# Kernel optimization log

Hardware: AMD Instinct MI355X
Metric: run time of the kernel (lower is better)

## Reference

```python
import jax, jax.numpy as jnp
import numpy as np

# Constants from the torch module __init__
FACE_INDS = np.array([[0, 1, 2, 3], [0, 4, 2, 6], [0, 1, 4, 5],
                      [1, 3, 5, 7], [2, 3, 6, 7], [4, 5, 6, 7]])  # (6,4)
N_GRID = 11
N_POINTS = N_GRID * N_GRID        # 121
N_FACE = 6
N_KP_HAND = 21
N_CONTACTS = 10
ITA = 0.2
IND1 = np.array([0, 1, 2, 3])
IND2 = np.array([1, 2, 3, 0])


def _bilinear_grid():
    # grid[p, k] = bilinear weights for the 4 face corners, p over 11x11 (u,v)
    g = []
    for u in np.linspace(0.0, 1.0, N_GRID):
        for v in np.linspace(0.0, 1.0, N_GRID):
            g.append([v * (1 - u), v * u, (1 - v) * (1 - u), u * (1 - v)])
    return jnp.asarray(np.array(g, dtype=np.float32))  # (121, 4)


def setup_inputs() -> dict:
    key = jax.random.key(0)
    poses = jax.random.normal(key, (8192, N_KP_HAND + 8, 3), dtype=jnp.float32)
    return {"poses": poses}


def affinity_loss(poses):
    bs = poses.shape[0]
    hand = poses[:, :N_KP_HAND, :]          # (bs, 21, 3)
    obj = poses[:, N_KP_HAND:, :]           # (bs, 8, 3)

    # --- sample_face_points: bilinear sample 121 pts on each of the 6 faces ---
    grid = _bilinear_grid().astype(poses.dtype)        # (121, 4)
    faces = obj[:, FACE_INDS, :]                        # (bs, 6, 4, 3)
    face_points = jnp.einsum('bfkc,pk->bfpc', faces, grid)  # (bs, 6, 121, 3)
    obj_pts = face_points.reshape(bs, N_FACE * N_POINTS, 3)  # (bs, 726, 3)

    xx = jnp.sum(hand * hand, axis=-1)                  # (bs, 21)
    yy = jnp.sum(obj_pts * obj_pts, axis=-1)            # (bs, 726)
    zz = jnp.einsum('bic,bjc->bij', hand, obj_pts)      # (bs, 21, 726)
    pdist = jnp.sqrt(xx[:, :, None] + yy[:, None, :] - 2.0 * zz + 1e-6)
    pdist = pdist.reshape(bs, N_KP_HAND, N_FACE, N_POINTS)

    # --- per (hand kp, face) nearest face point, then global top-10 contacts ---
    dist_h2f = jnp.min(pdist, axis=3)                   # (bs, 21, 6)
    idxs_h2f = jnp.argmin(pdist, axis=3)                # (bs, 21, 6)
    flat = dist_h2f.reshape(bs, N_KP_HAND * N_FACE)     # (bs, 126)
    order = jnp.argsort(flat, axis=1)[:, :N_CONTACTS]   # (bs, 10)
    dist = jnp.take_along_axis(flat, order, axis=1)     # (bs, 10)
    inds_hand = order // N_FACE
    inds_face = order % N_FACE
    b = jnp.arange(bs)[:, None]
    ind_obj = idxs_h2f[b, inds_hand, inds_face]                     # (bs, 10)
    obj_contacts = obj_pts[b, inds_face * N_POINTS + ind_obj]       # (bs, 10, 3)

    # --- get_obj_info: axis endpoints and mean edge length of the bbox ---
    points1 = obj[:, :4, :].mean(axis=1)                # (bs, 3)
    points2 = obj[:, 4:, :].mean(axis=1)                # (bs, 3)
    l1 = jnp.linalg.norm(obj[:, IND1] - obj[:, IND2], axis=-1).mean(1, keepdims=True)
    l2 = jnp.linalg.norm(obj[:, IND1 + 4] - obj[:, IND2 + 4], axis=-1).mean(1, keepdims=True)
    length = (l1 + l2) * 0.5                            # (bs, 1)

    mask1 = (dist < length * ITA).astype(poses.dtype)   # (bs, 10)
    mask = mask1[:, :, None] * mask1[:, None, :]        # (bs, 10, 10)

    direct_vec = points2 - points1                      # (bs, 3)
    dv_norm = jnp.linalg.norm(direct_vec, axis=1, keepdims=True)  # (bs, 1)
    normed_dv = direct_vec / (dv_norm + 1e-5)
    vec_contacts = obj_contacts - points1[:, None, :]   # (bs, 10, 3)
    inner = jnp.sum(direct_vec[:, None, :] * vec_contacts, axis=-1)  # (bs, 10)
    t = inner / (dv_norm + 1e-5)                        # (bs, 10)
    r = points1[:, None, :] + normed_dv[:, None, :] * t[:, :, None]  # (bs, 10, 3)
    normal_vec = obj_contacts - r
    normal_vec = normal_vec / (jnp.linalg.norm(normal_vec, axis=2, keepdims=True) + 1e-5)
    cos_sim = jnp.einsum('bic,bjc->bij', normal_vec, normal_vec)  # (bs, 10, 10)

    return (cos_sim * mask).sum() / (mask.sum() + 1.0)


def reference(poses):
    return affinity_loss(poses)
```

## Files before the change

### kernel.cpp

```cpp
#include <hip/hip_runtime.h>
#include <math.h>

#define NGRID   11
#define NPAIR   126
#define NCONT   10

#define NSUB    64
#define NBUK    128
#define WS_SUB  16
#define WS_BUK  128
#define WS_WORDS (WS_BUK + 2 * NBUK)

#define NBUCKET 256

__device__ __constant__ int4 c_face4[6] = {
    {0,1,2,3},{0,4,2,6},{0,1,4,5},{1,3,5,7},{2,3,6,7},{4,5,6,7}};
__device__ __constant__ float c_U[NGRID] = {
    0.0f,0.1f,0.2f,0.3f,0.4f,0.5f,0.6f,0.7f,0.8f,0.9f,1.0f};

__global__ void zero_ws_kernel(float* ws, int n) {
    int t = blockIdx.x * 256 + threadIdx.x;
    if (t < n) ws[t] = 0.0f;
}

__device__ __forceinline__ void pair_coefs(
        const float* __restrict__ obj, float hx, float hy, float hz, int f,
        float& C00, float& C10, float& C01, float& C11,
        float& C20, float& C02, float& C21, float& C12, float& C22) {
    const int4 F = c_face4[f];
    float C0[3], C1[3], C2[3], C3[3];
    #pragma unroll
    for (int c = 0; c < 3; ++c) {
        C0[c] = obj[F.x * 3 + c];
        C1[c] = obj[F.y * 3 + c];
        C2[c] = obj[F.z * 3 + c];
        C3[c] = obj[F.w * 3 + c];
    }
    float av[3], bv[3], cv[3], dv[3];
    #pragma unroll
    for (int c = 0; c < 3; ++c) {
        av[c] = C2[c];
        bv[c] = C3[c] - C2[c];
        cv[c] = C0[c] - C2[c];
        dv[c] = C1[c] - C0[c] - C3[c] + C2[c];
    }
    float aa = 0.f, bb = 0.f, cc = 0.f, dd = 0.f;
    float ab = 0.f, ac = 0.f, ad = 0.f, bc = 0.f, bd = 0.f, cd = 0.f;
    #pragma unroll
    for (int c = 0; c < 3; ++c) {
        aa += av[c] * av[c]; bb += bv[c] * bv[c];
        cc += cv[c] * cv[c]; dd += dv[c] * dv[c];
        ab += av[c] * bv[c]; ac += av[c] * cv[c];
        ad += av[c] * dv[c]; bc += bv[c] * cv[c];
        bd += bv[c] * dv[c]; cd += cv[c] * dv[c];
    }
    const float hx2 = 2.0f * hx, hy2 = 2.0f * hy, hz2 = 2.0f * hz;
    const float ha2 = fmaf(hx2, av[0], fmaf(hy2, av[1], hz2 * av[2]));
    const float hb2 = fmaf(hx2, bv[0], fmaf(hy2, bv[1], hz2 * bv[2]));
    const float hc2 = fmaf(hx2, cv[0], fmaf(hy2, cv[1], hz2 * cv[2]));
    const float hd2 = fmaf(hx2, dv[0], fmaf(hy2, dv[1], hz2 * dv[2]));
    C00 = ha2 - aa;
    C10 = hb2 - 2.f * ab;
    C01 = hc2 - 2.f * ac;
    C11 = hd2 - 2.f * (ad + bc);
    C20 = -bb;  C02 = -cc;  C21 = -2.f * bd;  C12 = -2.f * cd;  C22 = -dd;
}

__launch_bounds__(256)
__global__ void affinity_kernel(const float* __restrict__ poses,
                                float* __restrict__ ws,
                                float* __restrict__ out,
                                int bs, int mode) {
    const int t    = threadIdx.x;
    const int half = t >> 7;
    const int t0   = t & 127;
    const int batch = blockIdx.x * 2 + half;
    const bool valid = batch < bs;

    __shared__ float sh_pose[2][88];
    __shared__ __align__(16) unsigned sh_key[2][128];
    __shared__ int   sh_ru[2][128];
    __shared__ int   sh_ch[2][NCONT];
    __shared__ float sh_ctr[2][NCONT][4];
    __shared__ float sh_nd[2][2];
    __shared__ int    sh_last;
    __shared__ double sh_rn[4], sh_rd[4];

    if (valid && t0 < 87) sh_pose[half][t0] = poses[(size_t)batch * 87 + t0];
    __syncthreads();

    const float* hand = sh_pose[half];
    const float* obj  = sh_pose[half] + 63;

    if (t0 >= NPAIR) sh_key[half][t0] = 0xFFFFFFFFu;
    if (valid && t0 < NPAIR) {
        const int i = t0 / 6;
        const int f = t0 - i * 6;
        const float hx = hand[i * 3 + 0], hy = hand[i * 3 + 1], hz = hand[i * 3 + 2];
        const float xx = hx * hx + hy * hy + hz * hz;
        float C00, C10, C01, C11, C20, C02, C21, C12, C22;
        pair_coefs(obj, hx, hy, hz, f, C00, C10, C01, C11, C20, C02, C21, C12, C22);

        const float U[NGRID] = {0.0f,0.1f,0.2f,0.3f,0.4f,0.5f,
                                0.6f,0.7f,0.8f,0.9f,1.0f};
        float qb = -3.0e38f;
        int   ru = 0;
        #pragma unroll
        for (int iu = 0; iu < NGRID; ++iu) {
            const float u  = U[iu];
            const float A2 = fmaf(fmaf(C22, u, C12), u, C02);
            const float A1 = fmaf(fmaf(C21, u, C11), u, C01);
            const float A0 = fmaf(fmaf(C20, u, C10), u, C00);
            float qr = A0;
            #pragma unroll
            for (int iv = 1; iv < NGRID; ++iv) {
                qr = fmaxf(qr, fmaf(fmaf(A2, U[iv], A1), U[iv], A0));
            }
            if (qr > qb) { qb = qr; ru = iu; }
        }
        float d2 = fmaxf(xx - qb, 0.0f);
        sh_key[half][t0] = (__float_as_uint(d2) & 0xFFFFFF80u) | (unsigned)t0;
        sh_ru[half][t0]  = ru;
    }
    __syncthreads();

    if (valid && t0 < NPAIR) {
        const unsigned ki = sh_key[half][t0];
        const uint4* kp = (const uint4*)sh_key[half];
        int rank = 0;
        #pragma unroll 8
        for (int j = 0; j < 32; ++j) {
            const uint4 v = kp[j];
            rank += (v.x < ki) + (v.y < ki) + (v.z < ki) + (v.w < ki);
        }
        if (rank < NCONT) sh_ch[half][rank] = t0;
    }
    __syncthreads();

    if (valid && t0 < NCONT) {
        const int ci = sh_ch[half][t0];
        const int i  = ci / 6;
        const int f  = ci - 6 * i;
        const int ru = sh_ru[half][ci];
        const float hx = hand[i * 3 + 0], hy = hand[i * 3 + 1], hz = hand[i * 3 + 2];

        float C00, C10, C01, C11, C20, C02, C21, C12, C22;
        pair_coefs(obj, hx, hy, hz, f, C00, C10, C01, C11, C20, C02, C21, C12, C22);
        const float u  = c_U[ru];
        const float A2 = fmaf(fmaf(C22, u, C12), u, C02);
        const float A1 = fmaf(fmaf(C21, u, C11), u, C01);
        const float A0 = fmaf(fmaf(C20, u, C10), u, C00);
        const float U[NGRID] = {0.0f,0.1f,0.2f,0.3f,0.4f,0.5f,
                                0.6f,0.7f,0.8f,0.9f,1.0f};
        float qr = A0;
        int   vb = 0;
        #pragma unroll
        for (int iv = 1; iv < NGRID; ++iv) {
            const float q = fmaf(fmaf(A2, U[iv], A1), U[iv], A0);
            if (q > qr) { qr = q; vb = iv; }
        }

        const double du = ru * 0.1;
        const double dv = vb * 0.1;
        const float w0 = (float)(dv * (1.0 - du));
        const float w1 = (float)(dv * du);
        const float w2 = (float)((1.0 - dv) * (1.0 - du));
        const float w3 = (float)(du * (1.0 - dv));
        const int4 F = c_face4[f];
        const int i0 = F.x * 3, i1 = F.y * 3, i2 = F.z * 3, i3 = F.w * 3;
        const float cx = w0 * obj[i0 + 0] + w1 * obj[i1 + 0]
                       + w2 * obj[i2 + 0] + w3 * obj[i3 + 0];
        const float cy = w0 * obj[i0 + 1] + w1 * obj[i1 + 1]
                       + w2 * obj[i2 + 1] + w3 * obj[i3 + 1];
        const float cz = w0 * obj[i0 + 2] + w1 * obj[i1 + 2]
                       + w2 * obj[i2 + 2] + w3 * obj[i3 + 2];

        const float xx = hx * hx + hy * hy + hz * hz;
        const float yy = cx * cx + cy * cy + cz * cz;
        const float zz = hx * cx + hy * cy + hz * cz;
        const float dist = sqrtf(((xx + yy) - 2.0f * zz) + 1e-6f);

        float p1x = (((obj[0]  + obj[3])  + obj[6])  + obj[9])  * 0.25f;
        float p1y = (((obj[1]  + obj[4])  + obj[7])  + obj[10]) * 0.25f;
        float p1z = (((obj[2]  + obj[5])  + obj[8])  + obj[11]) * 0.25f;
        float p2x = (((obj[12] + obj[15]) + obj[18]) + obj[21]) * 0.25f;
        float p2y = (((obj[13] + obj[16]) + obj[19]) + obj[22]) * 0.25f;
        float p2z = (((obj[14] + obj[17]) + obj[20]) + obj[23]) * 0.25f;

        float l1 = 0.0f, l2 = 0.0f;
        #pragma unroll
        for (int e = 0; e < 4; ++e) {
            const int a = e, b2 = (e + 1) & 3;
            {
                const float dx = obj[a * 3 + 0] - obj[b2 * 3 + 0];
                const float dy = obj[a * 3 + 1] - obj[b2 * 3 + 1];
                const float dz = obj[a * 3 + 2] - obj[b2 * 3 + 2];
                l1 += sqrtf(dx * dx + dy * dy + dz * dz);
            }
            {
                const float dx = obj[(a + 4) * 3 + 0] - obj[(b2 + 4) * 3 + 0];
                const float dy = obj[(a + 4) * 3 + 1] - obj[(b2 + 4) * 3 + 1];
                const float dz = obj[(a + 4) * 3 + 2] - obj[(b2 + 4) * 3 + 2];
                l2 += sqrtf(dx * dx + dy * dy + dz * dz);
            }
        }
        l1 *= 0.25f; l2 *= 0.25f;
        const float length = (l1 + l2) * 0.5f;
        const float m = (dist < length * 0.2f) ? 1.0f : 0.0f;

        const float dvx = p2x - p1x, dvy = p2y - p1y, dvz = p2z - p1z;
        const float dvn = sqrtf(dvx * dvx + dvy * dvy + dvz * dvz);
        const float den = dvn + 1e-5f;
        const float ndx = dvx / den, ndy = dvy / den, ndz = dvz / den;
        const float vcx = cx - p1x, vcy = cy - p1y, vcz = cz - p1z;
        const float inner = dvx * vcx + dvy * vcy + dvz * vcz;
        const float tp = inner / den;
        const float rx = p1x + ndx * tp, ry = p1y + ndy * tp, rz = p1z + ndz * tp;
        float nvx = cx - rx, nvy = cy - ry, nvz = cz - rz;
        const float nvn = sqrtf(nvx * nvx + nvy * nvy + nvz * nvz) + 1e-5f;
        nvx /= nvn; nvy /= nvn; nvz /= nvn;

        sh_ctr[half][t0][0] = m * nvx;
        sh_ctr[half][t0][1] = m * nvy;
        sh_ctr[half][t0][2] = m * nvz;
        sh_ctr[half][t0][3] = m;
    }
    __syncthreads();

    if (t0 == 0) {
        float num = 0.f, dnm = 0.f;
        if (valid) {
            float sx = 0.f, sy = 0.f, sz = 0.f, sk = 0.f;
            #pragma unroll
            for (int c = 0; c < NCONT; ++c) {
                sx += sh_ctr[half][c][0]; sy += sh_ctr[half][c][1];
                sz += sh_ctr[half][c][2]; sk += sh_ctr[half][c][3];
            }
            num = sx * sx + sy * sy + sz * sz;
            dnm = sk * sk;
        }
        sh_nd[half][0] = num;
        sh_nd[half][1] = dnm;
    }
    __syncthreads();

    if (t == 0) {
        sh_last = 0;
        const float num = sh_nd[0][0] + sh_nd[1][0];
        const float dnm = sh_nd[0][1] + sh_nd[1][1];
        const int b = blockIdx.x;
        if (mode) {
            float* bkt = ws + WS_BUK + 2 * (b & (NBUK - 1));
            const float r0 = atomicAdd(bkt + 0, num);
            const float r1 = atomicAdd(bkt + 1, dnm);
            asm volatile("" :: "v"(r0), "v"(r1) : "memory");
            unsigned* subs = (unsigned*)ws + WS_SUB;
            const unsigned nb = gridDim.x;
            const unsigned g  = (unsigned)b & (NSUB - 1);
            const unsigned quota = (nb - 1u - g) / NSUB + 1u;
            const unsigned old = atomicAdd(subs + g, 1u);
            if (old + 1u == quota) {
                const unsigned ngroups = nb < NSUB ? nb : NSUB;
                const unsigned m2 = atomicAdd((unsigned*)ws, 1u);
                if (m2 + 1u == ngroups) sh_last = 1;
            }
        } else {
            float* bucket = ws + 2 * (b & (NBUCKET - 1));
            atomicAdd(bucket + 0, num);
            atomicAdd(bucket + 1, dnm);
        }
    }
    __syncthreads();

    if (sh_last) {
        double n = 0.0, d = 0.0;
        if (t < NBUK) {
            float* bkt = ws + WS_BUK + 2 * t;
            n = (double)atomicAdd(bkt + 0, 0.0f);
            d = (double)atomicAdd(bkt + 1, 0.0f);
        }
        #pragma unroll
        for (int off = 32; off >= 1; off >>= 1) {
            n += __shfl_xor(n, off, 64);
            d += __shfl_xor(d, off, 64);
        }
        const int w = t >> 6;
        if ((t & 63) == 0) { sh_rn[w] = n; sh_rd[w] = d; }
        __syncthreads();
        if (t == 0) {
            const double nn = sh_rn[0] + sh_rn[1] + sh_rn[2] + sh_rn[3];
            const double dd = sh_rd[0] + sh_rd[1] + sh_rd[2] + sh_rd[3];
            out[0] = (float)(nn / (dd + 1.0));
        }
    }
}

__launch_bounds__(1024)
__global__ void finalize_kernel(const float* __restrict__ ws,
                                float* __restrict__ out, int nslot) {
    const int t = threadIdx.x;
    __shared__ double sh_n[16], sh_d[16];
    double n = 0.0, d = 0.0;
    for (int k = t; k < nslot; k += 1024) {
        n += (double)ws[2 * k + 0];
        d += (double)ws[2 * k + 1];
    }
    #pragma unroll
    for (int off = 32; off >= 1; off >>= 1) {
        n += __shfl_xor(n, off, 64);
        d += __shfl_xor(d, off, 64);
    }
    const int w = t >> 6;
    if ((t & 63) == 0) { sh_n[w] = n; sh_d[w] = d; }
    __syncthreads();
    if (t == 0) {
        double nn = 0.0, dd = 0.0;
        #pragma unroll
        for (int i = 0; i < 16; ++i) { nn += sh_n[i]; dd += sh_d[i]; }
        out[0] = (float)(nn / (dd + 1.0));
    }
}

extern "C" void kernel_launch(void* const* d_in, const int* in_sizes, int n_in,
                              void* d_out, int out_size, void* d_ws, size_t ws_size,
                              hipStream_t stream) {
    const float* poses = (const float*)d_in[0];
    float* out = (float*)d_out;
    float* ws  = (float*)d_ws;
    const int bs = in_sizes[0] / 87;
    const int nblk = (bs + 1) / 2;

    if (ws_size >= (size_t)WS_WORDS * sizeof(float)) {
        hipMemsetAsync(ws, 0, WS_WORDS * sizeof(float), stream);
        hipLaunchKernelGGL(affinity_kernel, dim3(nblk), dim3(256), 0, stream,
                           poses, ws, out, bs, 1);
    } else {
        hipLaunchKernelGGL(zero_ws_kernel, dim3(1), dim3(256), 0, stream,
                           ws, NBUCKET * 2);
        hipLaunchKernelGGL(affinity_kernel, dim3(nblk), dim3(256), 0, stream,
                           poses, ws, out, bs, 0);
        hipLaunchKernelGGL(finalize_kernel, dim3(1), dim3(1024), 0, stream,
                           ws, out, NBUCKET);
    }
}
```

Baseline: 82.58 us.

## Precompute per-face coefficients, packed-FMA grid search, and threshold-filter contact candidates

Per-face quadratic coefficients are computed once per batch by six threads and stored in shared memory instead of being recomputed by every pair thread. The 11x11 grid scan now evaluates two u rows at a time with packed float2 FMA and max. Pairs whose approximate squared distance exceeds the contact threshold are dropped early, so only survivors get refined, ranked among themselves and reduced. The final sum uses a wavefront shuffle instead of a serial loop. The filter depends on a heuristic slack term and changes the ranking structure, which could affect correctness at threshold edges.

```diff
diff --git a/kernel.cpp b/kernel.cpp
--- a/kernel.cpp
+++ b/kernel.cpp
@@ -13,6 +13,11 @@
 
 #define NBUCKET 256
 
+typedef float v2f __attribute__((ext_vector_type(2)));
+#define FMA2(a,b,c) __builtin_elementwise_fma((a),(b),(c))
+#define MAX2(a,b)   __builtin_elementwise_max((a),(b))
+#define SP2(x)      ((v2f){(x),(x)})
+
 __device__ __constant__ int4 c_face4[6] = {
     {0,1,2,3},{0,4,2,6},{0,1,4,5},{1,3,5,7},{2,3,6,7},{4,5,6,7}};
 __device__ __constant__ float c_U[NGRID] = {
@@ -23,47 +28,22 @@
     if (t < n) ws[t] = 0.0f;
 }
 
-__device__ __forceinline__ void pair_coefs(
-        const float* __restrict__ obj, float hx, float hy, float hz, int f,
+__device__ __forceinline__ void coefs_from_face(
+        const float4* __restrict__ Ff, float hx, float hy, float hz,
         float& C00, float& C10, float& C01, float& C11,
         float& C20, float& C02, float& C21, float& C12, float& C22) {
-    const int4 F = c_face4[f];
-    float C0[3], C1[3], C2[3], C3[3];
-    #pragma unroll
-    for (int c = 0; c < 3; ++c) {
-        C0[c] = obj[F.x * 3 + c];
-        C1[c] = obj[F.y * 3 + c];
-        C2[c] = obj[F.z * 3 + c];
-        C3[c] = obj[F.w * 3 + c];
-    }
-    float av[3], bv[3], cv[3], dv[3];
-    #pragma unroll
-    for (int c = 0; c < 3; ++c) {
-        av[c] = C2[c];
-        bv[c] = C3[c] - C2[c];
-        cv[c] = C0[c] - C2[c];
-        dv[c] = C1[c] - C0[c] - C3[c] + C2[c];
-    }
-    float aa = 0.f, bb = 0.f, cc = 0.f, dd = 0.f;
-    float ab = 0.f, ac = 0.f, ad = 0.f, bc = 0.f, bd = 0.f, cd = 0.f;
-    #pragma unroll
-    for (int c = 0; c < 3; ++c) {
-        aa += av[c] * av[c]; bb += bv[c] * bv[c];
-        cc += cv[c] * cv[c]; dd += dv[c] * dv[c];
-        ab += av[c] * bv[c]; ac += av[c] * cv[c];
-        ad += av[c] * dv[c]; bc += bv[c] * cv[c];
-        bd += bv[c] * dv[c]; cd += cv[c] * dv[c];
-    }
+    const float4 F0 = Ff[0], F1 = Ff[1], F2 = Ff[2],
+                 F3 = Ff[3], F4 = Ff[4], F5 = Ff[5];
     const float hx2 = 2.0f * hx, hy2 = 2.0f * hy, hz2 = 2.0f * hz;
-    const float ha2 = fmaf(hx2, av[0], fmaf(hy2, av[1], hz2 * av[2]));
-    const float hb2 = fmaf(hx2, bv[0], fmaf(hy2, bv[1], hz2 * bv[2]));
-    const float hc2 = fmaf(hx2, cv[0], fmaf(hy2, cv[1], hz2 * cv[2]));
-    const float hd2 = fmaf(hx2, dv[0], fmaf(hy2, dv[1], hz2 * dv[2]));
-    C00 = ha2 - aa;
-    C10 = hb2 - 2.f * ab;
-    C01 = hc2 - 2.f * ac;
-    C11 = hd2 - 2.f * (ad + bc);
-    C20 = -bb;  C02 = -cc;  C21 = -2.f * bd;  C12 = -2.f * cd;  C22 = -dd;
+    const float ha2 = fmaf(hx2, F0.x, fmaf(hy2, F0.y, hz2 * F0.z));
+    const float hb2 = fmaf(hx2, F1.x, fmaf(hy2, F1.y, hz2 * F1.z));
+    const float hc2 = fmaf(hx2, F2.x, fmaf(hy2, F2.y, hz2 * F2.z));
+    const float hd2 = fmaf(hx2, F3.x, fmaf(hy2, F3.y, hz2 * F3.z));
+    C00 = ha2 - F0.w;
+    C10 = hb2 - F4.x;
+    C01 = hc2 - F4.y;
+    C11 = hd2 - F4.z;
+    C20 = -F1.w;  C02 = -F2.w;  C21 = -F4.w;  C12 = -F5.x;  C22 = -F3.w;
 }
 
 __launch_bounds__(256)
@@ -77,170 +57,234 @@
     const int batch = blockIdx.x * 2 + half;
     const bool valid = batch < bs;
 
-    __shared__ float sh_pose[2][88];
-    __shared__ __align__(16) unsigned sh_key[2][128];
-    __shared__ int   sh_ru[2][128];
-    __shared__ int   sh_ch[2][NCONT];
-    __shared__ float sh_ctr[2][NCONT][4];
-    __shared__ float sh_nd[2][2];
-    __shared__ int    sh_last;
-    __shared__ double sh_rn[4], sh_rd[4];
+    __shared__ float    sh_pose[2][88];
+    __shared__ float4   sh_face[2][36];
+    __shared__ float    sh_thr[2][2];
+    __shared__ int      sh_ru[2][128];
+    __shared__ int      sh_cpair[2][128];
+    __shared__ unsigned sh_cnt[2], sh_cnt2[2];
+    __shared__ unsigned sh_key[2][128];
+    __shared__ float    sh_cont[2][128][3];
+    __shared__ float    sh_win[2][NCONT][3];
+    __shared__ float    sh_nd[2][2];
+    __shared__ int      sh_last;
+    __shared__ double   sh_rn[4], sh_rd[4];
 
     if (valid && t0 < 87) sh_pose[half][t0] = poses[(size_t)batch * 87 + t0];
+    if (t0 == 127) { sh_cnt[half] = 0u; sh_cnt2[half] = 0u; }
     __syncthreads();
 
     const float* hand = sh_pose[half];
     const float* obj  = sh_pose[half] + 63;
 
-    if (t0 >= NPAIR) sh_key[half][t0] = 0xFFFFFFFFu;
+    if (valid && t0 < 6) {
+        const int4 F = c_face4[t0];
+        float C0[3], C1[3], C2[3], C3[3];
+        #pragma unroll
+        for (int c = 0; c < 3; ++c) {
+            C0[c] = obj[F.x * 3 + c];
+            C1[c] = obj[F.y * 3 + c];
+            C2[c] = obj[F.z * 3 + c];
+            C3[c] = obj[F.w * 3 + c];
+        }
+        float av[3], bv[3], cv[3], dv[3];
+        #pragma unroll
+        for (int c = 0; c < 3; ++c) {
+            av[c] = C2[c];
+            bv[c] = C3[c] - C2[c];
+            cv[c] = C0[c] - C2[c];
+            dv[c] = C1[c] - C0[c] - C3[c] + C2[c];
+        }
+        float aa=0.f,bb=0.f,cc=0.f,dd=0.f,ab=0.f,ac=0.f,ad=0.f,bc=0.f,bd=0.f,cd=0.f;
+        #pragma unroll
+        for (int c = 0; c < 3; ++c) {
+            aa += av[c]*av[c]; bb += bv[c]*bv[c];
+            cc += cv[c]*cv[c]; dd += dv[c]*dv[c];
+            ab += av[c]*bv[c]; ac += av[c]*cv[c];
+            ad += av[c]*dv[c]; bc += bv[c]*cv[c];
+            bd += bv[c]*dv[c]; cd += cv[c]*dv[c];
+        }
+        float4* Ff = &sh_face[half][t0 * 6];
+        Ff[0] = make_float4(av[0], av[1], av[2], aa);
+        Ff[1] = make_float4(bv[0], bv[1], bv[2], bb);
+        Ff[2] = make_float4(cv[0], cv[1], cv[2], cc);
+        Ff[3] = make_float4(dv[0], dv[1], dv[2], dd);
+        Ff[4] = make_float4(2.f*ab, 2.f*ac, 2.f*(ad+bc), 2.f*bd);
+        Ff[5] = make_float4(2.f*cd, 0.f, 0.f, 0.f);
+    }
+    if (valid && t0 == 6) {
+        float l1 = 0.0f, l2 = 0.0f;
+        #pragma unroll
+        for (int e = 0; e < 4; ++e) {
+            const int a = e, b2 = (e + 1) & 3;
+            {
+                const float dx = obj[a*3+0]-obj[b2*3+0];
+                const float dy = obj[a*3+1]-obj[b2*3+1];
+                const float dz = obj[a*3+2]-obj[b2*3+2];
+                l1 += sqrtf(dx*dx + dy*dy + dz*dz);
+            }
+            {
+                const float dx = obj[(a+4)*3+0]-obj[(b2+4)*3+0];
+                const float dy = obj[(a+4)*3+1]-obj[(b2+4)*3+1];
+                const float dz = obj[(a+4)*3+2]-obj[(b2+4)*3+2];
+                l2 += sqrtf(dx*dx + dy*dy + dz*dz);
+            }
+        }
+        l1 *= 0.25f; l2 *= 0.25f;
+        const float L02 = (l1 + l2) * 0.5f * 0.2f;
+        sh_thr[half][0] = L02 * L02 - 1e-6f + 1e-2f;
+        sh_thr[half][1] = L02;
+    }
+    __syncthreads();
+
     if (valid && t0 < NPAIR) {
         const int i = t0 / 6;
         const int f = t0 - i * 6;
-        const float hx = hand[i * 3 + 0], hy = hand[i * 3 + 1], hz = hand[i * 3 + 2];
-        const float xx = hx * hx + hy * hy + hz * hz;
-        float C00, C10, C01, C11, C20, C02, C21, C12, C22;
-        pair_coefs(obj, hx, hy, hz, f, C00, C10, C01, C11, C20, C02, C21, C12, C22);
+        const float hx = hand[i*3+0], hy = hand[i*3+1], hz = hand[i*3+2];
+        const float xx = hx*hx + hy*hy + hz*hz;
+        float C00,C10,C01,C11,C20,C02,C21,C12,C22;
+        coefs_from_face(&sh_face[half][f*6], hx, hy, hz,
+                        C00,C10,C01,C11,C20,C02,C21,C12,C22);
 
         const float U[NGRID] = {0.0f,0.1f,0.2f,0.3f,0.4f,0.5f,
                                 0.6f,0.7f,0.8f,0.9f,1.0f};
         float qb = -3.0e38f;
         int   ru = 0;
         #pragma unroll
-        for (int iu = 0; iu < NGRID; ++iu) {
-            const float u  = U[iu];
-            const float A2 = fmaf(fmaf(C22, u, C12), u, C02);
-            const float A1 = fmaf(fmaf(C21, u, C11), u, C01);
-            const float A0 = fmaf(fmaf(C20, u, C10), u, C00);
-            float qr = A0;
+        for (int rp = 0; rp < 5; ++rp) {
+            const v2f u2 = (v2f){U[2*rp], U[2*rp+1]};
+            const v2f A2 = FMA2(FMA2(SP2(C22), u2, SP2(C12)), u2, SP2(C02));
+            const v2f A1 = FMA2(FMA2(SP2(C21), u2, SP2(C11)), u2, SP2(C01));
+            const v2f A0 = FMA2(FMA2(SP2(C20), u2, SP2(C10)), u2, SP2(C00));
+            v2f m2 = A0;
             #pragma unroll
             for (int iv = 1; iv < NGRID; ++iv) {
-                qr = fmaxf(qr, fmaf(fmaf(A2, U[iv], A1), U[iv], A0));
-            }
-            if (qr > qb) { qb = qr; ru = iu; }
-        }
-        float d2 = fmaxf(xx - qb, 0.0f);
-        sh_key[half][t0] = (__float_as_uint(d2) & 0xFFFFFF80u) | (unsigned)t0;
-        sh_ru[half][t0]  = ru;
-    }
-    __syncthreads();
-
-    if (valid && t0 < NPAIR) {
-        const unsigned ki = sh_key[half][t0];
-        const uint4* kp = (const uint4*)sh_key[half];
+                const v2f vv = SP2(U[iv]);
+                m2 = MAX2(m2, FMA2(FMA2(A2, vv, A1), vv, A0));
+            }
+            if (m2.x > qb) { qb = m2.x; ru = 2*rp; }
+            if (m2.y > qb) { qb = m2.y; ru = 2*rp + 1; }
+        }
+        {
+            const float u = 1.0f;
+            const float A2 = fmaf(fmaf(C22,u,C12),u,C02);
+            const float A1 = fmaf(fmaf(C21,u,C11),u,C01);
+            const float A0 = fmaf(fmaf(C20,u,C10),u,C00);
+            float m1 = A0;
+            #pragma unroll
+            for (int iv = 1; iv < NGRID; ++iv)
+                m1 = fmaxf(m1, fmaf(fmaf(A2,U[iv],A1),U[iv],A0));
+            if (m1 > qb) { qb = m1; ru = 10; }
+        }
+        sh_ru[half][t0] = ru;
+        const float d2s = xx - qb;
+        if (d2s < sh_thr[half][0]) {
+            const unsigned s = atomicAdd(&sh_cnt[half], 1u);
+            sh_cpair[half][s] = t0;
+        }
+    }
+    __syncthreads();
+
+    {
+        const int cnt = (int)sh_cnt[half];
+        if (t0 < cnt) {
+            const int pair = sh_cpair[half][t0];
+            const int i  = pair / 6;
+            const int f  = pair - 6 * i;
+            const int ru = sh_ru[half][pair];
+            const float hx = hand[i*3+0], hy = hand[i*3+1], hz = hand[i*3+2];
+            float C00,C10,C01,C11,C20,C02,C21,C12,C22;
+            coefs_from_face(&sh_face[half][f*6], hx, hy, hz,
+                            C00,C10,C01,C11,C20,C02,C21,C12,C22);
+            const float u  = c_U[ru];
+            const float A2 = fmaf(fmaf(C22,u,C12),u,C02);
+            const float A1 = fmaf(fmaf(C21,u,C11),u,C01);
+            const float A0 = fmaf(fmaf(C20,u,C10),u,C00);
+            const float U[NGRID] = {0.0f,0.1f,0.2f,0.3f,0.4f,0.5f,
+                                    0.6f,0.7f,0.8f,0.9f,1.0f};
+            float qr = A0; int vb = 0;
+            #pragma unroll
+            for (int iv = 1; iv < NGRID; ++iv) {
+                const float q = fmaf(fmaf(A2,U[iv],A1),U[iv],A0);
+                if (q > qr) { qr = q; vb = iv; }
+            }
+            const double du = ru * 0.1;
+            const double dv = vb * 0.1;
+            const float w0 = (float)(dv * (1.0 - du));
+            const float w1 = (float)(dv * du);
+            const float w2 = (float)((1.0 - dv) * (1.0 - du));
+            const float w3 = (float)(du * (1.0 - dv));
+            const int4 F = c_face4[f];
+            const int i0 = F.x*3, i1 = F.y*3, i2 = F.z*3, i3 = F.w*3;
+            const float cx = w0*obj[i0+0]+w1*obj[i1+0]+w2*obj[i2+0]+w3*obj[i3+0];
+            const float cy = w0*obj[i0+1]+w1*obj[i1+1]+w2*obj[i2+1]+w3*obj[i3+1];
+            const float cz = w0*obj[i0+2]+w1*obj[i1+2]+w2*obj[i2+2]+w3*obj[i3+2];
+            const float xx = hx*hx + hy*hy + hz*hz;
+            const float yy = cx*cx + cy*cy + cz*cz;
+            const float zz = hx*cx + hy*cy + hz*cz;
+            const float d2e = (xx + yy) - 2.0f * zz;
+            const float dist = sqrtf(d2e + 1e-6f);
+            if (dist < sh_thr[half][1]) {
+                const unsigned s2 = atomicAdd(&sh_cnt2[half], 1u);
+                const float d2k = fmaxf(d2e, 0.0f);
+                sh_key[half][s2] = (__float_as_uint(d2k) & 0xFFFFFF80u)
+                                 | (unsigned)pair;
+                sh_cont[half][s2][0] = cx;
+                sh_cont[half][s2][1] = cy;
+                sh_cont[half][s2][2] = cz;
+            }
+        }
+    }
+    __syncthreads();
+
+    const int n2 = (int)sh_cnt2[half];
+    if (t0 < n2) {
+        const unsigned ke = sh_key[half][t0];
         int rank = 0;
-        #pragma unroll 8
-        for (int j = 0; j < 32; ++j) {
-            const uint4 v = kp[j];
-            rank += (v.x < ki) + (v.y < ki) + (v.z < ki) + (v.w < ki);
-        }
-        if (rank < NCONT) sh_ch[half][rank] = t0;
-    }
-    __syncthreads();
-
-    if (valid && t0 < NCONT) {
-        const int ci = sh_ch[half][t0];
-        const int i  = ci / 6;
-        const int f  = ci - 6 * i;
-        const int ru = sh_ru[half][ci];
-        const float hx = hand[i * 3 + 0], hy = hand[i * 3 + 1], hz = hand[i * 3 + 2];
-
-        float C00, C10, C01, C11, C20, C02, C21, C12, C22;
-        pair_coefs(obj, hx, hy, hz, f, C00, C10, C01, C11, C20, C02, C21, C12, C22);
-        const float u  = c_U[ru];
-        const float A2 = fmaf(fmaf(C22, u, C12), u, C02);
-        const float A1 = fmaf(fmaf(C21, u, C11), u, C01);
-        const float A0 = fmaf(fmaf(C20, u, C10), u, C00);
-        const float U[NGRID] = {0.0f,0.1f,0.2f,0.3f,0.4f,0.5f,
-                                0.6f,0.7f,0.8f,0.9f,1.0f};
-        float qr = A0;
-        int   vb = 0;
-        #pragma unroll
-        for (int iv = 1; iv < NGRID; ++iv) {
-            const float q = fmaf(fmaf(A2, U[iv], A1), U[iv], A0);
-            if (q > qr) { qr = q; vb = iv; }
-        }
-
-        const double du = ru * 0.1;
-        const double dv = vb * 0.1;
-        const float w0 = (float)(dv * (1.0 - du));
-        const float w1 = (float)(dv * du);
-        const float w2 = (float)((1.0 - dv) * (1.0 - du));
-        const float w3 = (float)(du * (1.0 - dv));
-        const int4 F = c_face4[f];
-        const int i0 = F.x * 3, i1 = F.y * 3, i2 = F.z * 3, i3 = F.w * 3;
-        const float cx = w0 * obj[i0 + 0] + w1 * obj[i1 + 0]
-                       + w2 * obj[i2 + 0] + w3 * obj[i3 + 0];
-        const float cy = w0 * obj[i0 + 1] + w1 * obj[i1 + 1]
-                       + w2 * obj[i2 + 1] + w3 * obj[i3 + 1];
-        const float cz = w0 * obj[i0 + 2] + w1 * obj[i1 + 2]
-                       + w2 * obj[i2 + 2] + w3 * obj[i3 + 2];
-
-        const float xx = hx * hx + hy * hy + hz * hz;
-        const float yy = cx * cx + cy * cy + cz * cz;
-        const float zz = hx * cx + hy * cy + hz * cz;
-        const float dist = sqrtf(((xx + yy) - 2.0f * zz) + 1e-6f);
-
-        float p1x = (((obj[0]  + obj[3])  + obj[6])  + obj[9])  * 0.25f;
-        float p1y = (((obj[1]  + obj[4])  + obj[7])  + obj[10]) * 0.25f;
-        float p1z = (((obj[2]  + obj[5])  + obj[8])  + obj[11]) * 0.25f;
-        float p2x = (((obj[12] + obj[15]) + obj[18]) + obj[21]) * 0.25f;
-        float p2y = (((obj[13] + obj[16]) + obj[19]) + obj[22]) * 0.25f;
-        float p2z = (((obj[14] + obj[17]) + obj[20]) + obj[23]) * 0.25f;
-
-        float l1 = 0.0f, l2 = 0.0f;
-        #pragma unroll
-        for (int e = 0; e < 4; ++e) {
-            const int a = e, b2 = (e + 1) & 3;
-            {
-                const float dx = obj[a * 3 + 0] - obj[b2 * 3 + 0];
-                const float dy = obj[a * 3 + 1] - obj[b2 * 3 + 1];
-                const float dz = obj[a * 3 + 2] - obj[b2 * 3 + 2];
-                l1 += sqrtf(dx * dx + dy * dy + dz * dz);
-            }
-            {
-                const float dx = obj[(a + 4) * 3 + 0] - obj[(b2 + 4) * 3 + 0];
-                const float dy = obj[(a + 4) * 3 + 1] - obj[(b2 + 4) * 3 + 1];
-                const float dz = obj[(a + 4) * 3 + 2] - obj[(b2 + 4) * 3 + 2];
-                l2 += sqrtf(dx * dx + dy * dy + dz * dz);
-            }
-        }
-        l1 *= 0.25f; l2 *= 0.25f;
-        const float length = (l1 + l2) * 0.5f;
-        const float m = (dist < length * 0.2f) ? 1.0f : 0.0f;
-
-        const float dvx = p2x - p1x, dvy = p2y - p1y, dvz = p2z - p1z;
-        const float dvn = sqrtf(dvx * dvx + dvy * dvy + dvz * dvz);
+        for (int j = 0; j < n2; ++j) rank += (sh_key[half][j] < ke) ? 1 : 0;
+        if (rank < NCONT) {
+            sh_win[half][rank][0] = sh_cont[half][t0][0];
+            sh_win[half][rank][1] = sh_cont[half][t0][1];
+            sh_win[half][rank][2] = sh_cont[half][t0][2];
+        }
+    }
+    __syncthreads();
+
+    const int kwin = n2 < NCONT ? n2 : NCONT;
+    float px = 0.f, py = 0.f, pz = 0.f;
+    if (valid && t0 < kwin) {
+        const float cx = sh_win[half][t0][0];
+        const float cy = sh_win[half][t0][1];
+        const float cz = sh_win[half][t0][2];
+        const float p1x = (((obj[0] +obj[3]) +obj[6]) +obj[9]) *0.25f;
+        const float p1y = (((obj[1] +obj[4]) +obj[7]) +obj[10])*0.25f;
+        const float p1z = (((obj[2] +obj[5]) +obj[8]) +obj[11])*0.25f;
+        const float p2x = (((obj[12]+obj[15])+obj[18])+obj[21])*0.25f;
+        const float p2y = (((obj[13]+obj[16])+obj[19])+obj[22])*0.25f;
+        const float p2z = (((obj[14]+obj[17])+obj[20])+obj[23])*0.25f;
+        const float dvx = p2x-p1x, dvy = p2y-p1y, dvz = p2z-p1z;
+        const float dvn = sqrtf(dvx*dvx + dvy*dvy + dvz*dvz);
         const float den = dvn + 1e-5f;
-        const float ndx = dvx / den, ndy = dvy / den, ndz = dvz / den;
-        const float vcx = cx - p1x, vcy = cy - p1y, vcz = cz - p1z;
-        const float inner = dvx * vcx + dvy * vcy + dvz * vcz;
+        const float ndx = dvx/den, ndy = dvy/den, ndz = dvz/den;
+        const float vcx = cx-p1x, vcy = cy-p1y, vcz = cz-p1z;
+        const float inner = dvx*vcx + dvy*vcy + dvz*vcz;
         const float tp = inner / den;
-        const float rx = p1x + ndx * tp, ry = p1y + ndy * tp, rz = p1z + ndz * tp;
-        float nvx = cx - rx, nvy = cy - ry, nvz = cz - rz;
-        const float nvn = sqrtf(nvx * nvx + nvy * nvy + nvz * nvz) + 1e-5f;
-        nvx /= nvn; nvy /= nvn; nvz /= nvn;
-
-        sh_ctr[half][t0][0] = m * nvx;
-        sh_ctr[half][t0][1] = m * nvy;
-        sh_ctr[half][t0][2] = m * nvz;
-        sh_ctr[half][t0][3] = m;
-    }
-    __syncthreads();
-
-    if (t0 == 0) {
-        float num = 0.f, dnm = 0.f;
-        if (valid) {
-            float sx = 0.f, sy = 0.f, sz = 0.f, sk = 0.f;
-            #pragma unroll
-            for (int c = 0; c < NCONT; ++c) {
-                sx += sh_ctr[half][c][0]; sy += sh_ctr[half][c][1];
-                sz += sh_ctr[half][c][2]; sk += sh_ctr[half][c][3];
-            }
-            num = sx * sx + sy * sy + sz * sz;
-            dnm = sk * sk;
-        }
-        sh_nd[half][0] = num;
-        sh_nd[half][1] = dnm;
+        const float rx = p1x + ndx*tp, ry = p1y + ndy*tp, rz = p1z + ndz*tp;
+        float nvx = cx-rx, nvy = cy-ry, nvz = cz-rz;
+        const float nvn = sqrtf(nvx*nvx + nvy*nvy + nvz*nvz) + 1e-5f;
+        px = nvx / nvn; py = nvy / nvn; pz = nvz / nvn;
+    }
+    if (t0 < 64) {
+        #pragma unroll
+        for (int off = 32; off >= 1; off >>= 1) {
+            px += __shfl_xor(px, off, 64);
+            py += __shfl_xor(py, off, 64);
+            pz += __shfl_xor(pz, off, 64);
+        }
+        if (t0 == 0) {
+            sh_nd[half][0] = px*px + py*py + pz*pz;
+            sh_nd[half][1] = (float)(kwin * kwin);
+        }
     }
     __syncthreads();
 
```

Measured after the change: 77.21 us. 1.07x faster.
